# Kernel optimization log

Hardware: AMD Instinct MI355X
Metric: run time of the kernel (lower is better)

## Reference

```python
import jax, jax.numpy as jnp
import numpy as np

NUM_CODES = 1024
CODE_DIM = 64
EMA_DECAY = 0.99
COMMIT_W = 0.25
EPS = 1e-5
B = 262144


def setup_inputs() -> dict:
    key = jax.random.key(0)
    k1, k2, k3, k4 = jax.random.split(key, 4)
    z = jax.random.normal(k1, (B, CODE_DIM), dtype=jnp.float32)
    weight = jax.random.normal(k2, (NUM_CODES, CODE_DIM), dtype=jnp.float32)
    ema_cluster_size = jax.random.uniform(k3, (NUM_CODES,), dtype=jnp.float32)
    ema_embed_sum = jax.random.normal(k4, (NUM_CODES, CODE_DIM), dtype=jnp.float32)
    return {"z": z, "weight": weight, "ema_cluster_size": ema_cluster_size,
            "ema_embed_sum": ema_embed_sum}


def reference(z, weight, ema_cluster_size, ema_embed_sum):
    # Squared Euclidean distances (argmin equivalent to cdist argmin)
    # d2[b,k] = ||z_b||^2 - 2 z_b . w_k + ||w_k||^2
    z2 = jnp.sum(z * z, axis=-1, keepdims=True)          # (B, 1)
    w2 = jnp.sum(weight * weight, axis=-1)               # (K,)
    d2 = z2 - 2.0 * (z @ weight.T) + w2[None, :]         # (B, K)
    indices = jnp.argmin(d2, axis=-1)                    # (B,)
    z_q = weight[indices]                                # gather with OLD weights

    # EMA codebook update (training, ema_update=True)
    ones = jnp.ones((z.shape[0],), dtype=z.dtype)
    cluster_size = jax.ops.segment_sum(ones, indices, num_segments=NUM_CODES)
    embed_sum = jax.ops.segment_sum(z, indices, num_segments=NUM_CODES)
    new_cs = EMA_DECAY * ema_cluster_size + (1.0 - EMA_DECAY) * cluster_size
    new_es = EMA_DECAY * ema_embed_sum + (1.0 - EMA_DECAY) * embed_sum
    n = jnp.sum(new_cs)
    smoothed = (new_cs + EPS) / (n + NUM_CODES * EPS) * n
    new_weight = new_es / smoothed[:, None]

    # commitment loss (z detached in torch; pure value here)
    vq_loss = COMMIT_W * jnp.mean((z - z_q) ** 2)

    # straight-through estimator
    z_q_st = z + jax.lax.stop_gradient(z_q - z)
    return z_q_st, indices, vq_loss, new_cs, new_es, new_weight
```

## Files before the change

### kernel.cpp

```cpp
#include <hip/hip_runtime.h>

typedef __attribute__((ext_vector_type(8))) short bf16x8;
typedef __attribute__((ext_vector_type(4))) float f32x4;

#define B_ROWS 262144
#define K_CODES 1024
#define DIM 64
#define SDELTA 0.015f

#define OUT_ZQ 0
#define OUT_IDX 16777216
#define OUT_LOSS 17039360
#define OUT_NEWCS 17039361
#define OUT_NEWES 17040385
#define OUT_NEWW 17105921

#define WS_LOSS   0
#define WS_QCOUNT 1
#define WS_W2     16
#define WS_SMOOTH 1040
#define WS_WHIP   2064
#define WS_WLOP   34832
#define WS_CPART  67600
#define WS_EPART  100368
#define WS_MINI   2197520
#define WS_QUEUE  2459664

static __device__ __forceinline__ unsigned short f2bf(float x) {
    unsigned u = __float_as_uint(x);
    return (unsigned short)((u + 0x7fffu + ((u >> 16) & 1u)) >> 16);
}
static __device__ __forceinline__ float bf2f(unsigned short u) {
    return __uint_as_float(((unsigned)u) << 16);
}

static __device__ __forceinline__ float red16(float x) {
    int v;
    v = __builtin_amdgcn_update_dpp(0, __float_as_int(x), 0x128, 0xF, 0xF, true);
    x += __int_as_float(v);
    v = __builtin_amdgcn_update_dpp(0, __float_as_int(x), 0x124, 0xF, 0xF, true);
    x += __int_as_float(v);
    v = __builtin_amdgcn_update_dpp(0, __float_as_int(x), 0x122, 0xF, 0xF, true);
    x += __int_as_float(v);
    v = __builtin_amdgcn_update_dpp(0, __float_as_int(x), 0x121, 0xF, 0xF, true);
    x += __int_as_float(v);
    return x;
}

static __device__ __forceinline__ void cvt_frag(const float* zrow, bf16x8& hi, bf16x8& lo) {
    float4 f0 = *(const float4*)zrow;
    float4 f1 = *(const float4*)(zrow + 4);
    float tf[8] = {f0.x, f0.y, f0.z, f0.w, f1.x, f1.y, f1.z, f1.w};
#pragma unroll
    for (int j = 0; j < 8; ++j) {
        unsigned short h = f2bf(tf[j]);
        hi[j] = (short)h;
        lo[j] = (short)f2bf(tf[j] - bf2f(h));
    }
}

__global__ __launch_bounds__(256) void vq_prep(const float* __restrict__ w,
                                               float* __restrict__ ws) {
    int b = blockIdx.x, tid = threadIdx.x;
    if (b < 4) {
        int k = b * 256 + tid;
        const float4* w4 = (const float4*)(w + (size_t)k * DIM);
        float s = 0.f;
#pragma unroll
        for (int j = 0; j < 16; ++j) {
            float4 v = w4[j];
            s += v.x * v.x + v.y * v.y + v.z * v.z + v.w * v.w;
        }
        ws[WS_W2 + k] = s;
    } else {
        int i = (b - 4) * 256 + tid;
        int p = i & 1023, c = i >> 10;
        int code = c * 128 + ((p >> 7) << 4) + (p & 15);
        int octet = ((p >> 6) & 1) * 4 + ((p >> 4) & 3);
        const float* src = w + (size_t)code * DIM + octet * 8;
        float4 f0 = *(const float4*)src;
        float4 f1 = *(const float4*)(src + 4);
        float tf[8] = {f0.x, f0.y, f0.z, f0.w, f1.x, f1.y, f1.z, f1.w};
        bf16x8 hv, lv;
#pragma unroll
        for (int j = 0; j < 8; ++j) {
            unsigned short hb = f2bf(tf[j]);
            hv[j] = (short)hb;
            lv[j] = (short)f2bf(tf[j] - bf2f(hb));
        }
        ((bf16x8*)(ws + WS_WHIP))[i] = hv;
        ((bf16x8*)(ws + WS_WLOP))[i] = lv;
    }
}

__global__ __launch_bounds__(256)
__attribute__((amdgpu_waves_per_eu(3, 4))) void vq_screen_kernel(
    const float* __restrict__ z, float* __restrict__ ws) {
    __shared__ float lds_w2h[K_CODES];

    int tid = threadIdx.x;
    int l = tid & 63, wave = tid >> 6;
    int m = l & 15, q = l >> 4;

    {
        float4 wv = ((const float4*)(ws + WS_W2))[tid];
        float4 hv;
        hv.x = -0.5f * wv.x;
        hv.y = -0.5f * wv.y;
        hv.z = -0.5f * wv.z;
        hv.w = -0.5f * wv.w;
        *(float4*)&lds_w2h[tid * 4] = hv;
    }

    int rowbase = blockIdx.x * 128 + wave * 32;
    bf16x8 zhi[2][2], zlo[2][2];
#pragma unroll
    for (int g = 0; g < 2; ++g) {
        const float* zr = z + (size_t)(rowbase + g * 16 + m) * DIM + q * 8;
        cvt_frag(zr, zhi[g][0], zlo[g][0]);
        cvt_frag(zr + 32, zhi[g][1], zlo[g][1]);
    }

    float kv[2], k2[2];
    kv[0] = kv[1] = -3.4e38f;
    k2[0] = k2[1] = -3.4e38f;

    const bf16x8* __restrict__ gh = (const bf16x8*)(ws + WS_WHIP);
    const bf16x8* __restrict__ gl = (const bf16x8*)(ws + WS_WLOP);

    __syncthreads();

    for (int cch = 0; cch < 8; ++cch) {
#pragma unroll 2
        for (int tg = 0; tg < 8; ++tg) {
            int gi = cch * 1024 + tg * 128 + l;
            bf16x8 bh0 = gh[gi];
            bf16x8 bh1 = gh[gi + 64];
            bf16x8 bl0 = gl[gi];
            bf16x8 bl1 = gl[gi + 64];
            unsigned cbase = (unsigned)(cch * 128 + tg * 16 + q * 4);
            unsigned ibase = (unsigned)((cch * 8 + tg) * 4);
            f32x4 cinit = *(const f32x4*)&lds_w2h[cbase];
#pragma unroll
            for (int g = 0; g < 2; ++g) {
                f32x4 acc = cinit;
                acc = __builtin_amdgcn_mfma_f32_16x16x32_bf16(bh0, zlo[g][0], acc, 0, 0, 0);
                acc = __builtin_amdgcn_mfma_f32_16x16x32_bf16(bl0, zhi[g][0], acc, 0, 0, 0);
                acc = __builtin_amdgcn_mfma_f32_16x16x32_bf16(bh1, zlo[g][1], acc, 0, 0, 0);
                acc = __builtin_amdgcn_mfma_f32_16x16x32_bf16(bl1, zhi[g][1], acc, 0, 0, 0);
                acc = __builtin_amdgcn_mfma_f32_16x16x32_bf16(bh0, zhi[g][0], acc, 0, 0, 0);
                acc = __builtin_amdgcn_mfma_f32_16x16x32_bf16(bh1, zhi[g][1], acc, 0, 0, 0);
                float a0 = __uint_as_float((__float_as_uint(acc[0]) & 0xFFFFFF00u) | ibase);
                float a1 = __uint_as_float((__float_as_uint(acc[1]) & 0xFFFFFF00u) | (ibase + 1u));
                float a2 = __uint_as_float((__float_as_uint(acc[2]) & 0xFFFFFF00u) | (ibase + 2u));
                float a3 = __uint_as_float((__float_as_uint(acc[3]) & 0xFFFFFF00u) | (ibase + 3u));
                float m01 = fmaxf(a0, a1), n01 = fminf(a0, a1);
                float m23 = fmaxf(a2, a3), n23 = fminf(a2, a3);
                float top = fmaxf(m01, m23);
                float sec = fmaxf(fmaxf(fminf(m01, m23), n01), n23);
                k2[g] = fmaxf(fmaxf(k2[g], sec), fminf(kv[g], top));
                kv[g] = fmaxf(kv[g], top);
            }
        }
    }

    float mv[2], m2[2];
    int mi[2];
#pragma unroll
    for (int g = 0; g < 2; ++g) {
        unsigned kb = __float_as_uint(kv[g]);
        unsigned i8 = kb & 255u;
        mi[g] = (int)((i8 >> 5) * 128 + ((i8 >> 2) & 7) * 16 + (unsigned)q * 4 + (i8 & 3));
        mv[g] = __uint_as_float(kb & 0xFFFFFF00u);
        m2[g] = __uint_as_float(__float_as_uint(k2[g]) & 0xFFFFFF00u);
    }
#pragma unroll
    for (int o = 16; o < 64; o <<= 1) {
#pragma unroll
        for (int g = 0; g < 2; ++g) {
            float ov = __shfl_xor(mv[g], o, 64);
            float ov2 = __shfl_xor(m2[g], o, 64);
            int oi = __shfl_xor(mi[g], o, 64);
            float nm2 = fmaxf(fmaxf(m2[g], ov2), fminf(mv[g], ov));
            bool take = (ov > mv[g]) || (ov == mv[g] && oi < mi[g]);
            mv[g] = take ? ov : mv[g];
            mi[g] = take ? oi : mi[g];
            m2[g] = nm2;
        }
    }
    if (q == 0) {
#pragma unroll
        for (int g = 0; g < 2; ++g) {
            bool amb = (mv[g] - m2[g]) <= SDELTA;
            ((int*)ws)[WS_MINI + rowbase + g * 16 + m] = mi[g] | (amb ? 0x80000000 : 0);
        }
    }
}

__global__ __launch_bounds__(256) void vq_gather_kernel(
    const float* __restrict__ z, const float* __restrict__ w,
    float* __restrict__ ws, float* __restrict__ out) {
    __shared__ float lred[4];
    int tid = threadIdx.x;
    int lane = tid & 63, wave = tid >> 6;
    int rsub = lane >> 4;
    int d4 = lane & 15;
    int wavebase = blockIdx.x * 256 + wave * 64;

    int encv[16];
#pragma unroll
    for (int s = 0; s < 16; ++s)
        encv[s] = ((const int*)ws)[WS_MINI + wavebase + s * 4 + rsub];

    float lsum = 0.f;
#pragma unroll
    for (int s = 0; s < 16; ++s) {
        int row = wavebase + s * 4 + rsub;
        int enc = encv[s];
        if (enc >= 0) {
            float4 x = ((const float4*)(z + (size_t)row * DIM))[d4];
            float4 qv = ((const float4*)(w + (size_t)enc * DIM))[d4];
            float4 st;
            st.x = x.x + (qv.x - x.x);
            st.y = x.y + (qv.y - x.y);
            st.z = x.z + (qv.z - x.z);
            st.w = x.w + (qv.w - x.w);
            ((float4*)(out + OUT_ZQ + (size_t)row * DIM))[d4] = st;
            float e0 = x.x - qv.x, e1 = x.y - qv.y, e2 = x.z - qv.z, e3 = x.w - qv.w;
            lsum += e0 * e0;
            lsum += e1 * e1;
            lsum += e2 * e2;
            lsum += e3 * e3;
            if (d4 == 0) out[OUT_IDX + row] = (float)enc;
        } else if (d4 == 0) {
            int pos = atomicAdd((int*)ws + WS_QCOUNT, 1);
            ((int*)ws)[WS_QUEUE + pos] = row;
        }
    }
#pragma unroll
    for (int o = 32; o; o >>= 1) lsum += __shfl_down(lsum, o, 64);
    if (lane == 0) lred[wave] = lsum;
    __syncthreads();
    if (tid == 0) atomicAdd(ws + WS_LOSS, lred[0] + lred[1] + lred[2] + lred[3]);
}

__global__ __launch_bounds__(256) void vq_fixup_kernel(
    const float* __restrict__ z, const float* __restrict__ w,
    float* __restrict__ ws, float* __restrict__ out) {
    const float* __restrict__ w2 = ws + WS_W2;
    __shared__ float sdd[4][4];
    __shared__ int sbi[4][4];
    int count = ((const int*)ws)[WS_QCOUNT];
    int tid = threadIdx.x;
    int lane = tid & 63, wave = tid >> 6;
    int sub = lane >> 4, d4 = lane & 15;
    float lacc = 0.f;
    for (int q0 = blockIdx.x * 4; q0 < count; q0 += gridDim.x * 4) {
        int qi = q0 + sub;
        bool active = qi < count;
        int row = ((const int*)ws)[WS_QUEUE + (active ? qi : 0)];
        float4 zx = ((const float4*)(z + (size_t)row * DIM))[d4];
        float zp = zx.x * zx.x;
        zp = fmaf(zx.y, zx.y, zp);
        zp = fmaf(zx.z, zx.z, zp);
        zp = fmaf(zx.w, zx.w, zp);
        float z2 = red16(zp);
        float best = 3.4e38f;
        int bi = 0;
        int c0 = wave * 256;
#pragma unroll 4
        for (int cc = 0; cc < 256; ++cc) {
            int c = c0 + cc;
            float4 wv4 = ((const float4*)(w + (size_t)c * DIM))[d4];
            float p = zx.x * wv4.x;
            p = fmaf(zx.y, wv4.y, p);
            p = fmaf(zx.z, wv4.z, p);
            p = fmaf(zx.w, wv4.w, p);
            p = red16(p);
            float dd = (z2 - 2.f * p) + w2[c];
            if (dd < best) { best = dd; bi = c; }
        }
        if (d4 == 0) { sdd[wave][sub] = best; sbi[wave][sub] = bi; }
        __syncthreads();
        if (wave == 0 && active) {
            float fb = sdd[0][sub];
            int fbi = sbi[0][sub];
#pragma unroll
            for (int v = 1; v < 4; ++v) {
                float od = sdd[v][sub];
                int oi = sbi[v][sub];
                if (od < fb || (od == fb && oi < fbi)) { fb = od; fbi = oi; }
            }
            float4 qv = ((const float4*)(w + (size_t)fbi * DIM))[d4];
            float4 st;
            st.x = zx.x + (qv.x - zx.x);
            st.y = zx.y + (qv.y - zx.y);
            st.z = zx.z + (qv.z - zx.z);
            st.w = zx.w + (qv.w - zx.w);
            ((float4*)(out + OUT_ZQ + (size_t)row * DIM))[d4] = st;
            float e0 = zx.x - qv.x, e1 = zx.y - qv.y;
            float e2 = zx.z - qv.z, e3 = zx.w - qv.w;
            float ls = e0 * e0 + e1 * e1 + e2 * e2 + e3 * e3;
            ls = red16(ls);
            if (d4 == 0) {
                out[OUT_IDX + row] = (float)fbi;
                lacc += ls;
            }
        }
        __syncthreads();
    }
    lacc += __shfl_xor(lacc, 16, 64);
    lacc += __shfl_xor(lacc, 32, 64);
    if (tid == 0 && lacc != 0.f) atomicAdd(ws + WS_LOSS, lacc);
}

__global__ __launch_bounds__(1024) void vq_embed_kernel(
    const float* __restrict__ z, const float* __restrict__ idx_f,
    float* __restrict__ ws) {
    __shared__ float eacc[128 * DIM];
    __shared__ float ecnt[128];
    __shared__ int lists[16][256];
    int b = blockIdx.x;
    int cs = b & 7, rs = b >> 3;
    float lo = (float)(cs * 128), hi = lo + 128.f;
    int tid = threadIdx.x;
    int wave = tid >> 6, lane = tid & 63;

#pragma unroll
    for (int j = 0; j < 8; ++j) eacc[j * 1024 + tid] = 0.f;
    if (tid < 128) ecnt[tid] = 0.f;
    __syncthreads();

    const float4* idx4 = (const float4*)idx_f;
    unsigned long long lanebits = (1ull << lane) - 1ull;
    for (int it = 0; it < 2; ++it) {
        int base = rs * 8192 + wave * 512 + it * 256;
        float4 f = idx4[(base >> 2) + lane];
        int cnt = 0;
#pragma unroll
        for (int c = 0; c < 4; ++c) {
            float fv = (c == 0) ? f.x : (c == 1) ? f.y : (c == 2) ? f.z : f.w;
            bool match = (fv >= lo && fv < hi);
            unsigned long long mmask = __ballot(match);
            if (match) {
                int pos = cnt + __popcll(mmask & lanebits);
                int row = base + 4 * lane + c;
                int local = (int)fv - cs * 128;
                lists[wave][pos] = (row << 7) | local;
                atomicAdd(&ecnt[local], 1.f);
            }
            cnt += __popcll(mmask);
        }
        int j = 0;
        for (; j + 4 <= cnt; j += 4) {
            int e0 = lists[wave][j], e1 = lists[wave][j + 1];
            int e2 = lists[wave][j + 2], e3 = lists[wave][j + 3];
            float v0 = z[(size_t)(e0 >> 7) * DIM + lane];
            float v1 = z[(size_t)(e1 >> 7) * DIM + lane];
            float v2 = z[(size_t)(e2 >> 7) * DIM + lane];
            float v3 = z[(size_t)(e3 >> 7) * DIM + lane];
            atomicAdd(&eacc[(e0 & 127) * DIM + lane], v0);
            atomicAdd(&eacc[(e1 & 127) * DIM + lane], v1);
            atomicAdd(&eacc[(e2 & 127) * DIM + lane], v2);
            atomicAdd(&eacc[(e3 & 127) * DIM + lane], v3);
        }
        for (; j < cnt; ++j) {
            int e = lists[wave][j];
            float v = z[(size_t)(e >> 7) * DIM + lane];
            atomicAdd(&eacc[(e & 127) * DIM + lane], v);
        }
    }
    __syncthreads();
#pragma unroll
    for (int j = 0; j < 8; ++j)
        ws[WS_EPART + (size_t)b * 8192 + j * 1024 + tid] = eacc[j * 1024 + tid];
    if (tid < 128) ws[WS_CPART + b * 128 + tid] = ecnt[tid];
}

__global__ __launch_bounds__(1024) void vq_finalize1_kernel(
    const float* __restrict__ ema_cs, float* __restrict__ ws,
    float* __restrict__ out) {
    int k = threadIdx.x;
    int cs = k >> 7, local = k & 127;
    float c = 0.f;
#pragma unroll
    for (int rs = 0; rs < 32; ++rs) c += ws[WS_CPART + (rs * 8 + cs) * 128 + local];
    float nc = 0.99f * ema_cs[k] + 0.01f * c;
    out[OUT_NEWCS + k] = nc;

    float s = nc;
#pragma unroll
    for (int o = 32; o; o >>= 1) s += __shfl_down(s, o, 64);
    __shared__ float red[16];
    __shared__ float n_sh;
    if ((k & 63) == 0) red[k >> 6] = s;
    __syncthreads();
    if (k == 0) {
        float n = 0.f;
#pragma unroll
        for (int i = 0; i < 16; ++i) n += red[i];
        n_sh = n;
        out[OUT_LOSS] = 0.25f * (ws[WS_LOSS] / 16777216.0f);
    }
    __syncthreads();
    float n = n_sh;
    ws[WS_SMOOTH + k] = (nc + 1e-5f) / (n + 0.01024f) * n;
}

__global__ __launch_bounds__(256) void vq_finalize2_kernel(
    const float* __restrict__ ema_es, const float* __restrict__ ws,
    float* __restrict__ out) {
    int i = blockIdx.x * 256 + threadIdx.x;
    int code = i >> 6, dim = i & 63;
    int cs = code >> 7, local = code & 127;
    float e = 0.f;
#pragma unroll
    for (int rs = 0; rs < 32; ++rs)
        e += ws[WS_EPART + (size_t)(rs * 8 + cs) * 8192 + local * DIM + dim];
    float es = 0.99f * ema_es[i] + 0.01f * e;
    out[OUT_NEWES + i] = es;
    out[OUT_NEWW + i] = es / ws[WS_SMOOTH + code];
}

extern "C" void kernel_launch(void* const* d_in, const int* in_sizes, int n_in,
                              void* d_out, int out_size, void* d_ws, size_t ws_size,
                              hipStream_t stream) {
    const float* z = (const float*)d_in[0];
    const float* weight = (const float*)d_in[1];
    const float* ema_cs = (const float*)d_in[2];
    const float* ema_es = (const float*)d_in[3];
    float* out = (float*)d_out;
    float* ws = (float*)d_ws;

    hipMemsetAsync(ws, 0, 64, stream);
    vq_prep<<<36, 256, 0, stream>>>(weight, ws);
    vq_screen_kernel<<<B_ROWS / 128, 256, 0, stream>>>(z, ws);
    vq_gather_kernel<<<B_ROWS / 256, 256, 0, stream>>>(z, weight, ws, out);
    vq_fixup_kernel<<<512, 256, 0, stream>>>(z, weight, ws, out);
    vq_embed_kernel<<<256, 1024, 0, stream>>>(z, out + OUT_IDX, ws);
    vq_finalize1_kernel<<<1, 1024, 0, stream>>>(ema_cs, ws, out);
    vq_finalize2_kernel<<<256, 256, 0, stream>>>(ema_es, ws, out);
}
```

Baseline: 396.3 us.

## Split embed segment-sum by dimension quarter instead of code range

The embed-sum kernel is repartitioned. Each block now accumulates all 1024 codes for a 16-dimension quarter of its row slice, instead of a 128-code range across all 64 dimensions. This removes the ballot/compaction lists and cuts the redundant index scans from 8x to 4x per row. The two finalize kernels' partial-sum indexing is updated to match. In exchange, grid size halves to 128 blocks, z is read in 64-byte chunks rather than full rows, and LDS use grows to about 68KB per block.

```diff
diff --git a/kernel.cpp b/kernel.cpp
--- a/kernel.cpp
+++ b/kernel.cpp
@@ -317,74 +317,44 @@
 __global__ __launch_bounds__(1024) void vq_embed_kernel(
     const float* __restrict__ z, const float* __restrict__ idx_f,
     float* __restrict__ ws) {
-    __shared__ float eacc[128 * DIM];
-    __shared__ float ecnt[128];
-    __shared__ int lists[16][256];
+    __shared__ float eacc[K_CODES * 16];
+    __shared__ float scnt[K_CODES];
     int b = blockIdx.x;
-    int cs = b & 7, rs = b >> 3;
-    float lo = (float)(cs * 128), hi = lo + 128.f;
+    int rs = b >> 2, q = b & 3;
     int tid = threadIdx.x;
-    int wave = tid >> 6, lane = tid & 63;
-
-#pragma unroll
-    for (int j = 0; j < 8; ++j) eacc[j * 1024 + tid] = 0.f;
-    if (tid < 128) ecnt[tid] = 0.f;
-    __syncthreads();
-
-    const float4* idx4 = (const float4*)idx_f;
-    unsigned long long lanebits = (1ull << lane) - 1ull;
-    for (int it = 0; it < 2; ++it) {
-        int base = rs * 8192 + wave * 512 + it * 256;
-        float4 f = idx4[(base >> 2) + lane];
-        int cnt = 0;
-#pragma unroll
-        for (int c = 0; c < 4; ++c) {
-            float fv = (c == 0) ? f.x : (c == 1) ? f.y : (c == 2) ? f.z : f.w;
-            bool match = (fv >= lo && fv < hi);
-            unsigned long long mmask = __ballot(match);
-            if (match) {
-                int pos = cnt + __popcll(mmask & lanebits);
-                int row = base + 4 * lane + c;
-                int local = (int)fv - cs * 128;
-                lists[wave][pos] = (row << 7) | local;
-                atomicAdd(&ecnt[local], 1.f);
-            }
-            cnt += __popcll(mmask);
-        }
-        int j = 0;
-        for (; j + 4 <= cnt; j += 4) {
-            int e0 = lists[wave][j], e1 = lists[wave][j + 1];
-            int e2 = lists[wave][j + 2], e3 = lists[wave][j + 3];
-            float v0 = z[(size_t)(e0 >> 7) * DIM + lane];
-            float v1 = z[(size_t)(e1 >> 7) * DIM + lane];
-            float v2 = z[(size_t)(e2 >> 7) * DIM + lane];
-            float v3 = z[(size_t)(e3 >> 7) * DIM + lane];
-            atomicAdd(&eacc[(e0 & 127) * DIM + lane], v0);
-            atomicAdd(&eacc[(e1 & 127) * DIM + lane], v1);
-            atomicAdd(&eacc[(e2 & 127) * DIM + lane], v2);
-            atomicAdd(&eacc[(e3 & 127) * DIM + lane], v3);
-        }
-        for (; j < cnt; ++j) {
-            int e = lists[wave][j];
-            float v = z[(size_t)(e >> 7) * DIM + lane];
-            atomicAdd(&eacc[(e & 127) * DIM + lane], v);
-        }
-    }
-    __syncthreads();
-#pragma unroll
-    for (int j = 0; j < 8; ++j)
-        ws[WS_EPART + (size_t)b * 8192 + j * 1024 + tid] = eacc[j * 1024 + tid];
-    if (tid < 128) ws[WS_CPART + b * 128 + tid] = ecnt[tid];
+    int lane = tid & 63, wave = tid >> 6;
+    int sub = lane >> 4, d = lane & 15;
+
+#pragma unroll
+    for (int j = 0; j < 16; ++j) eacc[j * 1024 + tid] = 0.f;
+    if (tid < 1024) scnt[tid] = 0.f;
+    __syncthreads();
+
+    int rbase = rs * 8192 + wave * 512 + sub;
+    const float* zq = z + q * 16 + d;
+#pragma unroll 4
+    for (int i = 0; i < 128; ++i) {
+        int row = rbase + i * 4;
+        float cf = idx_f[row];
+        float zv = zq[(size_t)row * DIM];
+        int code = (int)cf;
+        atomicAdd(&eacc[code * 16 + d], zv);
+        if (q == 0 && d == 0) atomicAdd(&scnt[code], 1.f);
+    }
+    __syncthreads();
+#pragma unroll
+    for (int j = 0; j < 16; ++j)
+        ws[WS_EPART + ((size_t)b * 16384) + j * 1024 + tid] = eacc[j * 1024 + tid];
+    if (q == 0) ws[WS_CPART + rs * 1024 + tid] = scnt[tid];
 }
 
 __global__ __launch_bounds__(1024) void vq_finalize1_kernel(
     const float* __restrict__ ema_cs, float* __restrict__ ws,
     float* __restrict__ out) {
     int k = threadIdx.x;
-    int cs = k >> 7, local = k & 127;
     float c = 0.f;
 #pragma unroll
-    for (int rs = 0; rs < 32; ++rs) c += ws[WS_CPART + (rs * 8 + cs) * 128 + local];
+    for (int rs = 0; rs < 32; ++rs) c += ws[WS_CPART + rs * 1024 + k];
     float nc = 0.99f * ema_cs[k] + 0.01f * c;
     out[OUT_NEWCS + k] = nc;
 
@@ -412,11 +382,11 @@
     float* __restrict__ out) {
     int i = blockIdx.x * 256 + threadIdx.x;
     int code = i >> 6, dim = i & 63;
-    int cs = code >> 7, local = code & 127;
+    int q = dim >> 4, d16 = dim & 15;
     float e = 0.f;
 #pragma unroll
     for (int rs = 0; rs < 32; ++rs)
-        e += ws[WS_EPART + (size_t)(rs * 8 + cs) * 8192 + local * DIM + dim];
+        e += ws[WS_EPART + (size_t)(rs * 4 + q) * 16384 + code * 16 + d16];
     float es = 0.99f * ema_es[i] + 0.01f * e;
     out[OUT_NEWES + i] = es;
     out[OUT_NEWW + i] = es / ws[WS_SMOOTH + code];
@@ -437,7 +407,7 @@
     vq_screen_kernel<<<B_ROWS / 128, 256, 0, stream>>>(z, ws);
     vq_gather_kernel<<<B_ROWS / 256, 256, 0, stream>>>(z, weight, ws, out);
     vq_fixup_kernel<<<512, 256, 0, stream>>>(z, weight, ws, out);
-    vq_embed_kernel<<<256, 1024, 0, stream>>>(z, out + OUT_IDX, ws);
+    vq_embed_kernel<<<128, 1024, 0, stream>>>(z, out + OUT_IDX, ws);
     vq_finalize1_kernel<<<1, 1024, 0, stream>>>(ema_cs, ws, out);
     vq_finalize2_kernel<<<256, 256, 0, stream>>>(ema_es, ws, out);
 }
```

Measured after the change: 452.8 us. +14.3%, slower.
